# Optimization experiments

Measured on AMD Instinct MI355X. Metric: run time of the kernel, lower is better.

## Reference

```python
import jax, jax.numpy as jnp
import numpy as np

L, B, D_IN, H = 1024, 64, 512, 512


def setup_inputs() -> dict:
    key = jax.random.key(0)
    ks = jax.random.split(key, 9)
    s = 1.0 / np.sqrt(H)
    inp = {
        "inputs": jax.random.normal(ks[0], (L, B, D_IN), dtype=jnp.float32),
        # canonical chain tree: node at step t is node t (left child = t-1)
        "indexes": jnp.broadcast_to(jnp.arange(L, dtype=jnp.int32)[:, None], (L, B)),
        # gate linears: ih has bias, lhh/rhh do not (per nn.Linear defs)
        "W_gih": jax.random.uniform(ks[1], (5 * H, D_IN), jnp.float32, -s, s),
        "b_gih": jax.random.uniform(ks[2], (5 * H,), jnp.float32, -s, s),
        "W_glhh": jax.random.uniform(ks[3], (5 * H, H), jnp.float32, -s, s),
        "W_grhh": jax.random.uniform(ks[4], (5 * H, H), jnp.float32, -s, s),
        "W_cih": jax.random.uniform(ks[5], (H, D_IN), jnp.float32, -s, s),
        "b_cih": jax.random.uniform(ks[6], (H,), jnp.float32, -s, s),
        "W_clhh": jax.random.uniform(ks[7], (H, H), jnp.float32, -s, s),
        "W_crhh": jax.random.uniform(ks[8], (H, H), jnp.float32, -s, s),
    }
    return inp


def _tree_gru(inputs, W_gih, b_gih, W_glhh, W_grhh, W_cih, b_cih, W_clhh, W_crhh):
    # chain tree: left_child_h = previous hidden, right_child_h = 0 (leaf side)
    batch = inputs.shape[1]
    hidden = W_clhh.shape[0]
    h0 = jnp.zeros((batch, hidden), inputs.dtype)

    def step(h_prev, x_t):
        left = h_prev
        right = jnp.zeros_like(h_prev)
        gates = jax.nn.sigmoid(
            x_t @ W_gih.T + b_gih + left @ W_glhh.T + right @ W_grhh.T
        )
        rl, rr, zl, zr, z = jnp.split(gates, 5, axis=1)
        cell = jnp.tanh(
            x_t @ W_cih.T + b_cih + (rl * left) @ W_clhh.T + (rr * right) @ W_crhh.T
        )
        h = zl * left + zr * right + z * cell  # node_forward hidden
        return h, h

    _, hs = jax.lax.scan(step, h0, inputs)  # hs: [L, B, H]
    outputs = jnp.transpose(hs, (1, 0, 2))  # [B, L, H], batch-first like original
    output_t = jnp.zeros((batch, hidden), inputs.dtype)  # original returns zeros
    return outputs, output_t


def reference(inputs, indexes, W_gih, b_gih, W_glhh, W_grhh, W_cih, b_cih,
              W_clhh, W_crhh):
    del indexes  # chain ordering: indexes[step, b] == step
    return _tree_gru(inputs, W_gih, b_gih, W_glhh, W_grhh,
                     W_cih, b_cih, W_clhh, W_crhh)
```

## Files before the change

kernel.cpp:

```cpp
#include <hip/hip_runtime.h>
#include <hip/hip_bf16.h>
#include <stdint.h>

typedef __bf16 bf16;
typedef __bf16 bf16x8 __attribute__((ext_vector_type(8)));
typedef __bf16 bf16x4 __attribute__((ext_vector_type(4)));
typedef float f32x16 __attribute__((ext_vector_type(16)));
typedef float f32x4 __attribute__((ext_vector_type(4)));

#define LL 1024
#define BB 64
#define HH 512
#define NR 8
#define NC 16
#define NWG (NR + NC)
#define NPROD 32
#define NLAUNCH (NWG + NPROD)
#define WSLOT 16
#define MFMA32(a, b, c) __builtin_amdgcn_mfma_f32_32x32x16_bf16(a, b, c, 0, 0, 0)

#define OFF_X      ((size_t)0)
#define OFF_WGSEL  ((size_t)67108864)
#define OFF_WCIH   ((size_t)68681728)
#define OFF_WHHZZ  ((size_t)69206016)
#define OFF_HBUF   ((size_t)70254592)
#define OFF_A2     ((size_t)70385664)
#define OFF_CTR    ((size_t)70516736)
#define OFF_XS     ((size_t)70517760)

static __device__ __forceinline__ float sigm(float x) {
  return 1.0f / (1.0f + __expf(-x));
}
static __device__ __forceinline__ float tanhx(float x) {
  x = fminf(15.0f, fmaxf(-15.0f, x));
  float e = __expf(2.0f * x);
  return (e - 1.0f) / (e + 1.0f);
}

static __device__ __forceinline__ unsigned ld_stamp(const unsigned* p) {
  unsigned s;
  asm volatile("global_load_dword %0, %1, off sc0 sc1\n\ts_waitcnt vmcnt(0)"
               : "=v"(s) : "v"(p) : "memory");
  return s;
}
static __device__ __forceinline__ void st_stamp(unsigned* p, unsigned v) {
  asm volatile("global_store_dword %0, %1, off sc0 sc1" :: "v"(p), "v"(v) : "memory");
}
static __device__ __forceinline__ void ld_frag(const bf16* p, bf16x8& d) {
  asm volatile("global_load_dwordx4 %0, %1, off sc0 sc1" : "=v"(d) : "v"(p) : "memory");
}
static __device__ __forceinline__ void ld_frag_c(const bf16* p, bf16x8& d) {
  asm volatile("global_load_dwordx4 %0, %1, off" : "=v"(d) : "v"(p) : "memory");
}
static __device__ __forceinline__ void ld_f4(const float* p, f32x4& d) {
  asm volatile("global_load_dwordx4 %0, %1, off sc0 sc1" : "=v"(d) : "v"(p) : "memory");
}
static __device__ __forceinline__ void st_f4(float* p, f32x4 v) {
  asm volatile("global_store_dwordx4 %0, %1, off sc0 sc1" :: "v"(p), "v"(v) : "memory");
}
static __device__ __forceinline__ void ld_u16(const bf16* p, unsigned& d) {
  asm volatile("global_load_ushort %0, %1, off sc0 sc1" : "=v"(d) : "v"(p) : "memory");
}
static __device__ __forceinline__ void st_u16(bf16* p, unsigned v) {
  asm volatile("global_store_short %0, %1, off sc0 sc1" :: "v"(p), "v"(v) : "memory");
}
#define VWAIT(n) do { asm volatile("s_waitcnt vmcnt(" #n ")" ::: "memory"); \
                      __builtin_amdgcn_sched_barrier(0); } while (0)

static __device__ __forceinline__ bf16x8 ldsfrag(const bf16* w, int i, int k) {
  unsigned byte = ((unsigned)i << 10) + ((unsigned)k << 1);
  byte ^= ((unsigned)(i & 7) << 4);
  return *(const bf16x8*)((const char*)w + byte);
}

__global__ __launch_bounds__(256) void k_cvt_x(const float* __restrict__ in,
                                               bf16* __restrict__ o) {
  size_t i = ((size_t)blockIdx.x * 256 + threadIdx.x) * 4;
  float4 f = *(const float4*)(in + i);
  bf16x4 v;
  v[0] = (bf16)f.x; v[1] = (bf16)f.y; v[2] = (bf16)f.z; v[3] = (bf16)f.w;
  *(bf16x4*)(o + i) = v;
}

__global__ __launch_bounds__(256) void k_cvt_w(const float* __restrict__ wgih,
                                               const float* __restrict__ wcf,
                                               const float* __restrict__ wglhh,
                                               bf16* __restrict__ wgsel,
                                               bf16* __restrict__ wcb,
                                               bf16* __restrict__ whhzz) {
  int i = blockIdx.x * 256 + threadIdx.x;
  const int NQ1 = (1536 * 512) / 4;
  const int NQ2 = (512 * 512) / 4;
  const float* s;
  bf16* d;
  if (i < NQ1) {
    int e = i * 4;
    int p = e >> 9, k = e & 511;
    int src = (p < 512) ? p : ((p < 1024) ? (1024 + p - 512) : (2048 + p - 1024));
    s = wgih + (size_t)src * 512 + k;
    d = wgsel + (size_t)p * 512 + k;
  } else if (i < NQ1 + NQ2) {
    int e = (i - NQ1) * 4;
    int n = e >> 9, k = e & 511;
    s = wcf + (size_t)n * 512 + k;
    d = wcb + (size_t)n * 512 + k;
  } else {
    int e = (i - NQ1 - NQ2) * 4;
    int q = e >> 9, k = e & 511;
    int src = (q < 512) ? (1024 + q) : (2048 + q - 512);
    s = wglhh + (size_t)src * 512 + k;
    d = whhzz + (size_t)q * 512 + k;
  }
  float4 f = *(const float4*)s;
  bf16x4 v;
  v[0] = (bf16)f.x; v[1] = (bf16)f.y; v[2] = (bf16)f.z; v[3] = (bf16)f.w;
  *(bf16x4*)d = v;
}

__global__ __launch_bounds__(256) void k_main(
    const bf16* __restrict__ xbf, const bf16* __restrict__ wgsel,
    const bf16* __restrict__ wcb, const bf16* __restrict__ whhzz,
    const float* __restrict__ wglhh, const float* __restrict__ wclhh,
    const float* __restrict__ bg, const float* __restrict__ bc,
    float* __restrict__ out, bf16* __restrict__ hbuf,
    bf16* __restrict__ a2buf, float* __restrict__ xs,
    unsigned* __restrict__ ctrs) {
  __shared__ __align__(16) char smem[64 * 1024];
  bf16* wlds = (bf16*)smem;
  float* zlzs = (float*)(smem + 32 * 1024);

  const int wg = blockIdx.x, tid = threadIdx.x;
  const int lane = tid & 63, wave = tid >> 6;
  const int lr = lane & 31, kq = (lane >> 5) * 8;
  unsigned* astamp = ctrs;
  unsigned* hstamp = ctrs + 16;
  unsigned* xstamp = ctrs + 64;

  if (wg >= NWG) {
    const int gx = (wg - NWG) * 4 + wave;
    const int proj = gx >> 5;
    const int m0 = 32 * ((gx >> 4) & 1);
    const int col = (gx & 15) * 32 + lr;
    float bias;
    const bf16* wb;
    if (proj == 0)      { bias = bg[col];        wb = wgsel + (size_t)col * HH; }
    else if (proj == 1) { bias = bg[1024 + col]; wb = wgsel + (size_t)(512 + col) * HH; }
    else if (proj == 2) { bias = bg[2048 + col]; wb = wgsel + (size_t)(1024 + col) * HH; }
    else                { bias = bc[col];        wb = wcb + (size_t)col * HH; }
    wb += kq;
    float* xsl = xs + ((size_t)gx * 64 + lane) * 16;
    for (int t = 0; t < LL; ++t) {
      if (t >= WSLOT) {
        const unsigned* sp = hstamp + (lane & 15);
        while (__any((int)(ld_stamp(sp) < (unsigned)(t - WSLOT + 1)))) {}
      }
      f32x16 a;
      #pragma unroll
      for (int r = 0; r < 16; ++r) a[r] = bias;
      const bf16* xa = xbf + (size_t)t * (BB * HH) + (size_t)(m0 + lr) * HH + kq;
      #pragma unroll 4
      for (int kk = 0; kk < 32; ++kk)
        a = MFMA32(*(const bf16x8*)(xa + kk * 16), *(const bf16x8*)(wb + kk * 16), a);
      float* dst = xsl + (size_t)(t & (WSLOT - 1)) * (128 * 64 * 16);
      f32x4 v0, v1, v2, v3;
      #pragma unroll
      for (int e = 0; e < 4; ++e) { v0[e] = a[e]; v1[e] = a[4 + e]; v2[e] = a[8 + e]; v3[e] = a[12 + e]; }
      st_f4(dst, v0); st_f4(dst + 4, v1); st_f4(dst + 8, v2); st_f4(dst + 12, v3);
      asm volatile("s_waitcnt vmcnt(0)" ::: "memory");
      if (lane == 0) st_stamp(xstamp + gx, (unsigned)(t + 1));
    }
    return;
  }
  __builtin_amdgcn_s_setprio(1);

  if (wg < NR) {
    const int m0 = 32 * (wave & 1);
    const int lc = 32 * (wave >> 1) + lr;
    const int p = wg * 64 + lc;
    const int mrow = m0 + 4 * (lane >> 5);
    const int gx = (wave & 1) * 16 + 2 * wg + (wave >> 1);

    for (int u = tid; u < 64 * 64; u += 256) {
      int i = u >> 6, k8 = (u & 63) << 3;
      const float* s = wglhh + (size_t)(wg * 64 + i) * HH + k8;
      bf16x8 v;
      #pragma unroll
      for (int j = 0; j < 8; ++j) v[j] = (bf16)s[j];
      unsigned byte = ((unsigned)i << 10) + ((unsigned)k8 << 1);
      byte ^= ((unsigned)(i & 7) << 4);
      *(bf16x8*)((char*)wlds + byte) = v;
    }
    __syncthreads();

    for (int t = 1; t < LL; ++t) {
      {
        const unsigned* sp = hstamp + (lane & 15);
        unsigned tgt = (unsigned)t;
        if (lane == 16) { sp = xstamp + gx; tgt = (unsigned)(t + 1); }
        while (__any((int)(ld_stamp(sp) < tgt))) {}
      }
      __builtin_amdgcn_sched_barrier(0);
      const float* xsp = xs + (((size_t)(t & (WSLOT - 1)) * 128 + gx) * 64 + lane) * 16;
      f32x4 xv0, xv1, xv2, xv3;
      ld_f4(xsp, xv0); ld_f4(xsp + 4, xv1); ld_f4(xsp + 8, xv2); ld_f4(xsp + 12, xv3);
      const bf16* hs = hbuf + (size_t)((t - 1) & 1) * (BB * HH);
      const bf16* ha = hs + (size_t)(m0 + lr) * HH + kq;
      bf16x8 fA[8], fB[8];
      unsigned hv[16];
      f32x16 acc;
      #pragma unroll
      for (int r = 0; r < 16; ++r) acc[r] = 0.0f;
      #pragma unroll
      for (int j = 0; j < 8; ++j) ld_frag(ha + j * 16, fA[j]);
      #pragma unroll
      for (int j = 0; j < 8; ++j) ld_frag(ha + (8 + j) * 16, fB[j]);
      VWAIT(8);
      #pragma unroll
      for (int j = 0; j < 8; ++j) acc = MFMA32(fA[j], ldsfrag(wlds, lc, j * 16 + kq), acc);
      #pragma unroll
      for (int j = 0; j < 8; ++j) ld_frag(ha + (16 + j) * 16, fA[j]);
      VWAIT(8);
      #pragma unroll
      for (int j = 0; j < 8; ++j) acc = MFMA32(fB[j], ldsfrag(wlds, lc, (8 + j) * 16 + kq), acc);
      #pragma unroll
      for (int j = 0; j < 8; ++j) ld_frag(ha + (24 + j) * 16, fB[j]);
      #pragma unroll
      for (int r = 0; r < 16; ++r) {
        int m = mrow + (r & 3) + 8 * (r >> 2);
        ld_u16(hs + (size_t)m * HH + p, hv[r]);
      }
      VWAIT(24);
      #pragma unroll
      for (int j = 0; j < 8; ++j) acc = MFMA32(fA[j], ldsfrag(wlds, lc, (16 + j) * 16 + kq), acc);
      VWAIT(16);
      #pragma unroll
      for (int j = 0; j < 8; ++j) acc = MFMA32(fB[j], ldsfrag(wlds, lc, (24 + j) * 16 + kq), acc);
      VWAIT(0);
      bf16* ad = a2buf + (size_t)(t & 1) * (BB * HH);
      #pragma unroll
      for (int r = 0; r < 16; ++r) {
        int m = mrow + (r & 3) + 8 * (r >> 2);
        float xadd = (r < 4) ? xv0[r & 3] : (r < 8) ? xv1[r & 3]
                   : (r < 12) ? xv2[r & 3] : xv3[r & 3];
        float gg = sigm(acc[r] + xadd);
        float hp = __builtin_bit_cast(float, hv[r] << 16);
        bf16 a = (bf16)(gg * hp);
        st_u16(ad + (size_t)m * HH + p, (unsigned)__builtin_bit_cast(unsigned short, a));
      }
      asm volatile("s_waitcnt vmcnt(0)" ::: "memory");
      __syncthreads();
      if (tid == 0) st_stamp(astamp + wg, (unsigned)(t + 1));
    }
  } else {
    const int cj = wg - NR;
    const int n = cj * 32 + lr;
    const bool crit = (wave < 2);
    const int m0 = crit ? 32 * wave : 32 * (wave - 2);
    const int mrow = m0 + 4 * (lane >> 5);
    const int Mq = (m0 >> 5) * 16;
    const int gc = 96 + Mq + cj;
    const int gzl = 32 + Mq + cj;
    const int gz = 64 + Mq + cj;

    for (int u = tid; u < 32 * 64; u += 256) {
      int i = u >> 6, k8 = (u & 63) << 3;
      const float* s = wclhh + (size_t)(cj * 32 + i) * HH + k8;
      bf16x8 v;
      #pragma unroll
      for (int j = 0; j < 8; ++j) v[j] = (bf16)s[j];
      unsigned byte = ((unsigned)i << 10) + ((unsigned)k8 << 1);
      byte ^= ((unsigned)(i & 7) << 4);
      *(bf16x8*)((char*)wlds + byte) = v;
    }
    __syncthreads();

    float hreg[16];
    #pragma unroll
    for (int r = 0; r < 16; ++r) hreg[r] = 0.0f;

    for (int t = 0; t < LL; ++t) {
      if (crit) {
        f32x16 acc, acc1;
        #pragma unroll
        for (int r = 0; r < 16; ++r) { acc[r] = 0.0f; acc1[r] = 0.0f; }
        f32x4 xv0, xv1, xv2, xv3;
        if (t > 0) {
          {
            const unsigned* sp = astamp + (lane & 7);
            unsigned tgt = (unsigned)(t + 1);
            if (lane == 8) sp = xstamp + gc;
            while (__any((int)(ld_stamp(sp) < tgt))) {}
          }
          __builtin_amdgcn_sched_barrier(0);
          const float* xsp = xs + (((size_t)(t & (WSLOT - 1)) * 128 + gc) * 64 + lane) * 16;
          ld_f4(xsp, xv0); ld_f4(xsp + 4, xv1); ld_f4(xsp + 8, xv2); ld_f4(xsp + 12, xv3);
          const bf16* aa = a2buf + (size_t)(t & 1) * (BB * HH) + (size_t)(m0 + lr) * HH + kq;
          bf16x8 fA[8], fB[8];
          #pragma unroll
          for (int j = 0; j < 8; ++j) ld_frag(aa + j * 16, fA[j]);
          #pragma unroll
          for (int j = 0; j < 8; ++j) ld_frag(aa + (8 + j) * 16, fB[j]);
          VWAIT(8);
          #pragma unroll
          for (int j = 0; j < 8; ++j) {
            if (j & 1) acc1 = MFMA32(fA[j], ldsfrag(wlds, lr, j * 16 + kq), acc1);
            else       acc  = MFMA32(fA[j], ldsfrag(wlds, lr, j * 16 + kq), acc);
          }
          #pragma unroll
          for (int j = 0; j < 8; ++j) ld_frag(aa + (16 + j) * 16, fA[j]);
          VWAIT(8);
          #pragma unroll
          for (int j = 0; j < 8; ++j) {
            if (j & 1) acc1 = MFMA32(fB[j], ldsfrag(wlds, lr, (8 + j) * 16 + kq), acc1);
            else       acc  = MFMA32(fB[j], ldsfrag(wlds, lr, (8 + j) * 16 + kq), acc);
          }
          #pragma unroll
          for (int j = 0; j < 8; ++j) ld_frag(aa + (24 + j) * 16, fB[j]);
          VWAIT(8);
          #pragma unroll
          for (int j = 0; j < 8; ++j) {
            if (j & 1) acc1 = MFMA32(fA[j], ldsfrag(wlds, lr, (16 + j) * 16 + kq), acc1);
            else       acc  = MFMA32(fA[j], ldsfrag(wlds, lr, (16 + j) * 16 + kq), acc);
          }
          VWAIT(0);
          #pragma unroll
          for (int j = 0; j < 8; ++j) {
            if (j & 1) acc1 = MFMA32(fB[j], ldsfrag(wlds, lr, (24 + j) * 16 + kq), acc1);
            else       acc  = MFMA32(fB[j], ldsfrag(wlds, lr, (24 + j) * 16 + kq), acc);
          }
        } else {
          {
            const unsigned* sp = xstamp + gc;
            while (__any((int)(ld_stamp(sp) < 1u))) {}
          }
          __builtin_amdgcn_sched_barrier(0);
          const float* xsp = xs + ((size_t)gc * 64 + lane) * 16;
          ld_f4(xsp, xv0); ld_f4(xsp + 4, xv1); ld_f4(xsp + 8, xv2); ld_f4(xsp + 12, xv3);
          VWAIT(0);
        }
        #pragma unroll
        for (int r = 0; r < 16; ++r) {
          float xadd = (r < 4) ? xv0[r & 3] : (r < 8) ? xv1[r & 3]
                     : (r < 12) ? xv2[r & 3] : xv3[r & 3];
          acc[r] += acc1[r] + xadd;
        }
        __syncthreads();
        bf16* hd = hbuf + (size_t)(t & 1) * (BB * HH);
        #pragma unroll
        for (int r = 0; r < 16; ++r) {
          int m = mrow + (r & 3) + 8 * (r >> 2);
          float zlv = zlzs[m * 32 + lr];
          float zv = zlzs[2048 + m * 32 + lr];
          float h = zlv * hreg[r] + zv * tanhx(acc[r]);
          hreg[r] = h;
          bf16 hb = (bf16)h;
          st_u16(hd + (size_t)m * HH + n, (unsigned)__builtin_bit_cast(unsigned short, hb));
        }
        asm volatile("s_waitcnt vmcnt(0)" ::: "memory");
      } else {
        f32x16 azl, az;
        #pragma unroll
        for (int r = 0; r < 16; ++r) { azl[r] = 0.0f; az[r] = 0.0f; }
        f32x4 l0, l1, l2, l3, z0, z1, z2, z3;
        if (t > 0) {
          {
            const unsigned* sp = hstamp + (lane & 15);
            unsigned tgt = (unsigned)t;
            if (lane == 16) { sp = xstamp + gzl; tgt = (unsigned)(t + 1); }
            if (lane == 17) { sp = xstamp + gz; tgt = (unsigned)(t + 1); }
            while (__any((int)(ld_stamp(sp) < tgt))) {}
          }
          __builtin_amdgcn_sched_barrier(0);
          const float* xl = xs + (((size_t)(t & (WSLOT - 1)) * 128 + gzl) * 64 + lane) * 16;
          const float* xz = xs + (((size_t)(t & (WSLOT - 1)) * 128 + gz) * 64 + lane) * 16;
          ld_f4(xl, l0); ld_f4(xl + 4, l1); ld_f4(xl + 8, l2); ld_f4(xl + 12, l3);
          ld_f4(xz, z0); ld_f4(xz + 4, z1); ld_f4(xz + 8, z2); ld_f4(xz + 12, z3);
          const bf16* hsA = hbuf + (size_t)((t - 1) & 1) * (BB * HH) + (size_t)(m0 + lr) * HH + kq;
          const bf16* bl = whhzz + (size_t)n * HH + kq;
          const bf16* bz = whhzz + (size_t)(512 + n) * HH + kq;
          bf16x8 A[2][4], Wl[2][4], Wz[2][4];
          #pragma unroll
          for (int j = 0; j < 4; ++j) {
            ld_frag(hsA + j * 16, A[0][j]);
            ld_frag_c(bl + j * 16, Wl[0][j]);
            ld_frag_c(bz + j * 16, Wz[0][j]);
          }
          #pragma unroll
          for (int b = 0; b < 8; ++b) {
            const int s = b & 1, ns = s ^ 1;
            if (b < 7) {
              #pragma unroll
              for (int j = 0; j < 4; ++j) {
                ld_frag(hsA + ((b + 1) * 4 + j) * 16, A[ns][j]);
                ld_frag_c(bl + ((b + 1) * 4 + j) * 16, Wl[ns][j]);
                ld_frag_c(bz + ((b + 1) * 4 + j) * 16, Wz[ns][j]);
              }
              VWAIT(12);
            } else {
              VWAIT(0);
            }
            #pragma unroll
            for (int j = 0; j < 4; ++j) {
              azl = MFMA32(A[s][j], Wl[s][j], azl);
              az = MFMA32(A[s][j], Wz[s][j], az);
            }
          }
        } else {
          {
            const unsigned* sp = xstamp + ((lane & 1) ? gz : gzl);
            while (__any((int)(ld_stamp(sp) < 1u))) {}
          }
          __builtin_amdgcn_sched_barrier(0);
          const float* xl = xs + ((size_t)gzl * 64 + lane) * 16;
          const float* xz = xs + ((size_t)gz * 64 + lane) * 16;
          ld_f4(xl, l0); ld_f4(xl + 4, l1); ld_f4(xl + 8, l2); ld_f4(xl + 12, l3);
          ld_f4(xz, z0); ld_f4(xz + 4, z1); ld_f4(xz + 8, z2); ld_f4(xz + 12, z3);
          VWAIT(0);
        }
        #pragma unroll
        for (int r = 0; r < 16; ++r) {
          int m = mrow + (r & 3) + 8 * (r >> 2);
          float xla = (r < 4) ? l0[r & 3] : (r < 8) ? l1[r & 3]
                    : (r < 12) ? l2[r & 3] : l3[r & 3];
          float xza = (r < 4) ? z0[r & 3] : (r < 8) ? z1[r & 3]
                    : (r < 12) ? z2[r & 3] : z3[r & 3];
          zlzs[m * 32 + lr] = sigm(azl[r] + xla);
          zlzs[2048 + m * 32 + lr] = sigm(az[r] + xza);
        }
        __syncthreads();
      }
      __syncthreads();
      if (tid == 0) st_stamp(hstamp + cj, (unsigned)(t + 1));
      if (crit) {
        #pragma unroll
        for (int r = 0; r < 16; ++r) {
          int m = mrow + (r & 3) + 8 * (r >> 2);
          out[(size_t)m * (LL * HH) + (size_t)t * HH + n] = hreg[r];
        }
      }
    }
  }
}

extern "C" void kernel_launch(void* const* d_in, const int* in_sizes, int n_in,
                              void* d_out, int out_size, void* d_ws, size_t ws_size,
                              hipStream_t stream) {
  (void)in_sizes; (void)n_in; (void)out_size; (void)ws_size;
  const float* x     = (const float*)d_in[0];
  const float* wgih  = (const float*)d_in[2];
  const float* bg    = (const float*)d_in[3];
  const float* wglhh = (const float*)d_in[4];
  const float* wcihf = (const float*)d_in[6];
  const float* bc    = (const float*)d_in[7];
  const float* wclhh = (const float*)d_in[8];
  float* out = (float*)d_out;

  char* ws = (char*)d_ws;
  bf16* xbf     = (bf16*)(ws + OFF_X);
  bf16* wgsel   = (bf16*)(ws + OFF_WGSEL);
  bf16* wcb     = (bf16*)(ws + OFF_WCIH);
  bf16* whhzz   = (bf16*)(ws + OFF_WHHZZ);
  bf16* hbuf    = (bf16*)(ws + OFF_HBUF);
  bf16* a2buf   = (bf16*)(ws + OFF_A2);
  float* xsb    = (float*)(ws + OFF_XS);
  unsigned* ctr = (unsigned*)(ws + OFF_CTR);

  hipMemsetAsync(ctr, 0, 1024, stream);
  hipMemsetAsync(out + (size_t)BB * LL * HH, 0, (size_t)BB * HH * sizeof(float), stream);

  k_cvt_x<<<dim3(32768), dim3(256), 0, stream>>>(x, xbf);
  k_cvt_w<<<dim3(1536), dim3(256), 0, stream>>>(wgih, wcihf, wglhh, wgsel, wcb, whhzz);
  k_main<<<dim3(NLAUNCH), dim3(256), 0, stream>>>(xbf, wgsel, wcb, whhzz, wglhh, wclhh,
                                                  bg, bc, out, hbuf, a2buf, xsb, ctr);
}
```

Baseline: 14.29 ms.

## Replace stamp-counter handshakes with per-element tagged hidden-state words

The hidden state and the gated product are now stored as 32-bit words, with the bf16 value in the high half and the step number in the low half. Consumers poll the data itself and retry only the fragments whose tags are stale, which replaces the separate stamp counters and the workgroup barrier plus stamp store on the producer side. This is meant to cut the cross-workgroup synchronisation latency on the serial recurrence path. In exchange it doubles the buffer footprint and global traffic per step, and adds unpacking ALU work and retry loops.

```diff
diff --git a/kernel.cpp b/kernel.cpp
--- a/kernel.cpp
+++ b/kernel.cpp
@@ -7,6 +7,8 @@
 typedef __bf16 bf16x4 __attribute__((ext_vector_type(4)));
 typedef float f32x16 __attribute__((ext_vector_type(16)));
 typedef float f32x4 __attribute__((ext_vector_type(4)));
+typedef unsigned u32;
+typedef unsigned u32x4 __attribute__((ext_vector_type(4)));
 
 #define LL 1024
 #define BB 64
@@ -24,9 +26,9 @@
 #define OFF_WCIH   ((size_t)68681728)
 #define OFF_WHHZZ  ((size_t)69206016)
 #define OFF_HBUF   ((size_t)70254592)
-#define OFF_A2     ((size_t)70385664)
-#define OFF_CTR    ((size_t)70516736)
-#define OFF_XS     ((size_t)70517760)
+#define OFF_A2     ((size_t)70516736)
+#define OFF_CTR    ((size_t)70778880)
+#define OFF_XS     ((size_t)70780928)
 
 static __device__ __forceinline__ float sigm(float x) {
   return 1.0f / (1.0f + __expf(-x));
@@ -46,8 +48,14 @@
 static __device__ __forceinline__ void st_stamp(unsigned* p, unsigned v) {
   asm volatile("global_store_dword %0, %1, off sc0 sc1" :: "v"(p), "v"(v) : "memory");
 }
-static __device__ __forceinline__ void ld_frag(const bf16* p, bf16x8& d) {
+static __device__ __forceinline__ void ld_d4(const u32* p, u32x4& d) {
   asm volatile("global_load_dwordx4 %0, %1, off sc0 sc1" : "=v"(d) : "v"(p) : "memory");
+}
+static __device__ __forceinline__ void ld_d1(const u32* p, u32& d) {
+  asm volatile("global_load_dword %0, %1, off sc0 sc1" : "=v"(d) : "v"(p) : "memory");
+}
+static __device__ __forceinline__ void st_d1(u32* p, u32 v) {
+  asm volatile("global_store_dword %0, %1, off sc0 sc1" :: "v"(p), "v"(v) : "memory");
 }
 static __device__ __forceinline__ void ld_frag_c(const bf16* p, bf16x8& d) {
   asm volatile("global_load_dwordx4 %0, %1, off" : "=v"(d) : "v"(p) : "memory");
@@ -58,14 +66,33 @@
 static __device__ __forceinline__ void st_f4(float* p, f32x4 v) {
   asm volatile("global_store_dwordx4 %0, %1, off sc0 sc1" :: "v"(p), "v"(v) : "memory");
 }
-static __device__ __forceinline__ void ld_u16(const bf16* p, unsigned& d) {
-  asm volatile("global_load_ushort %0, %1, off sc0 sc1" : "=v"(d) : "v"(p) : "memory");
-}
-static __device__ __forceinline__ void st_u16(bf16* p, unsigned v) {
-  asm volatile("global_store_short %0, %1, off sc0 sc1" :: "v"(p), "v"(v) : "memory");
-}
 #define VWAIT(n) do { asm volatile("s_waitcnt vmcnt(" #n ")" ::: "memory"); \
                       __builtin_amdgcn_sched_barrier(0); } while (0)
+
+#define PK2(a, b) (((a) >> 16) | ((b) & 0xFFFF0000u))
+static __device__ __forceinline__ bf16x8 frag_of(u32x4 a, u32x4 b) {
+  u32x4 p;
+  p[0] = PK2(a[0], a[1]); p[1] = PK2(a[2], a[3]);
+  p[2] = PK2(b[0], b[1]); p[3] = PK2(b[2], b[3]);
+  return __builtin_bit_cast(bf16x8, p);
+}
+static __device__ __forceinline__ bool bad4(u32x4 w, u32 et) {
+  return ((w[0] & 0xFFFFu) != et) | ((w[1] & 0xFFFFu) != et) |
+         ((w[2] & 0xFFFFu) != et) | ((w[3] & 0xFFFFu) != et);
+}
+static __device__ __forceinline__ void issue4(const u32* base, int g, u32x4* b) {
+  #pragma unroll
+  for (int j = 0; j < 4; ++j) {
+    ld_d4(base + (g * 4 + j) * 16, b[2 * j]);
+    ld_d4(base + (g * 4 + j) * 16 + 4, b[2 * j + 1]);
+  }
+}
+static __device__ __forceinline__ bool badbank(const u32x4* b, u32 et) {
+  bool bad = false;
+  #pragma unroll
+  for (int i = 0; i < 8; ++i) bad |= bad4(b[i], et);
+  return bad;
+}
 
 static __device__ __forceinline__ bf16x8 ldsfrag(const bf16* w, int i, int k) {
   unsigned byte = ((unsigned)i << 10) + ((unsigned)k << 1);
@@ -122,8 +149,8 @@
     const bf16* __restrict__ wcb, const bf16* __restrict__ whhzz,
     const float* __restrict__ wglhh, const float* __restrict__ wclhh,
     const float* __restrict__ bg, const float* __restrict__ bc,
-    float* __restrict__ out, bf16* __restrict__ hbuf,
-    bf16* __restrict__ a2buf, float* __restrict__ xs,
+    float* __restrict__ out, u32* __restrict__ hbuf32,
+    u32* __restrict__ a2buf32, float* __restrict__ xs,
     unsigned* __restrict__ ctrs) {
   __shared__ __align__(16) char smem[64 * 1024];
   bf16* wlds = (bf16*)smem;
@@ -132,7 +159,6 @@
   const int wg = blockIdx.x, tid = threadIdx.x;
   const int lane = tid & 63, wave = tid >> 6;
   const int lr = lane & 31, kq = (lane >> 5) * 8;
-  unsigned* astamp = ctrs;
   unsigned* hstamp = ctrs + 16;
   unsigned* xstamp = ctrs + 64;
 
@@ -193,63 +219,76 @@
     __syncthreads();
 
     for (int t = 1; t < LL; ++t) {
-      {
-        const unsigned* sp = hstamp + (lane & 15);
-        unsigned tgt = (unsigned)t;
-        if (lane == 16) { sp = xstamp + gx; tgt = (unsigned)(t + 1); }
-        while (__any((int)(ld_stamp(sp) < tgt))) {}
-      }
-      __builtin_amdgcn_sched_barrier(0);
+      const int par = (t - 1) & 1;
+      const u32 et = (u32)t;
+      const u32* hb = hbuf32 + (size_t)par * 32768 + (size_t)(m0 + lr) * 512 + kq;
+      const u32* hB = hbuf32 + (size_t)par * 32768;
+      u32x4 b0[8], b1[8];
+      u32 hv[16];
+      f32x16 acc;
+      #pragma unroll
+      for (int r = 0; r < 16; ++r) acc[r] = 0.0f;
+      f32x4 xv0, xv1, xv2, xv3;
+      bool xok = false;
+      for (;;) {
+        issue4(hb, 0, b0);
+        #pragma unroll
+        for (int r = 0; r < 16; ++r) {
+          int m = mrow + (r & 3) + 8 * (r >> 2);
+          ld_d1(hB + (size_t)m * 512 + p, hv[r]);
+        }
+        u32 xst = 0;
+        if (!xok) ld_d1((const u32*)(xstamp + gx), xst);
+        VWAIT(0);
+        if (!xok) xok = (xst >= (u32)(t + 1));
+        bool bad = badbank(b0, et);
+        #pragma unroll
+        for (int r = 0; r < 16; ++r) bad |= ((hv[r] & 0xFFFFu) != et);
+        if (!__any((int)bad)) break;
+      }
+      while (!xok) {
+        u32 xst;
+        ld_d1((const u32*)(xstamp + gx), xst);
+        VWAIT(0);
+        xok = (xst >= (u32)(t + 1));
+      }
       const float* xsp = xs + (((size_t)(t & (WSLOT - 1)) * 128 + gx) * 64 + lane) * 16;
-      f32x4 xv0, xv1, xv2, xv3;
       ld_f4(xsp, xv0); ld_f4(xsp + 4, xv1); ld_f4(xsp + 8, xv2); ld_f4(xsp + 12, xv3);
-      const bf16* hs = hbuf + (size_t)((t - 1) & 1) * (BB * HH);
-      const bf16* ha = hs + (size_t)(m0 + lr) * HH + kq;
-      bf16x8 fA[8], fB[8];
-      unsigned hv[16];
-      f32x16 acc;
-      #pragma unroll
-      for (int r = 0; r < 16; ++r) acc[r] = 0.0f;
-      #pragma unroll
-      for (int j = 0; j < 8; ++j) ld_frag(ha + j * 16, fA[j]);
-      #pragma unroll
-      for (int j = 0; j < 8; ++j) ld_frag(ha + (8 + j) * 16, fB[j]);
+      issue4(hb, 1, b1);
       VWAIT(8);
       #pragma unroll
-      for (int j = 0; j < 8; ++j) acc = MFMA32(fA[j], ldsfrag(wlds, lc, j * 16 + kq), acc);
-      #pragma unroll
-      for (int j = 0; j < 8; ++j) ld_frag(ha + (16 + j) * 16, fA[j]);
-      VWAIT(8);
-      #pragma unroll
-      for (int j = 0; j < 8; ++j) acc = MFMA32(fB[j], ldsfrag(wlds, lc, (8 + j) * 16 + kq), acc);
-      #pragma unroll
-      for (int j = 0; j < 8; ++j) ld_frag(ha + (24 + j) * 16, fB[j]);
-      #pragma unroll
-      for (int r = 0; r < 16; ++r) {
-        int m = mrow + (r & 3) + 8 * (r >> 2);
-        ld_u16(hs + (size_t)m * HH + p, hv[r]);
-      }
-      VWAIT(24);
-      #pragma unroll
-      for (int j = 0; j < 8; ++j) acc = MFMA32(fA[j], ldsfrag(wlds, lc, (16 + j) * 16 + kq), acc);
-      VWAIT(16);
-      #pragma unroll
-      for (int j = 0; j < 8; ++j) acc = MFMA32(fB[j], ldsfrag(wlds, lc, (24 + j) * 16 + kq), acc);
+      for (int j = 0; j < 4; ++j)
+        acc = MFMA32(frag_of(b0[2 * j], b0[2 * j + 1]), ldsfrag(wlds, lc, j * 16 + kq), acc);
+      #pragma unroll
+      for (int g = 1; g <= 6; ++g) {
+        u32x4* cur = (g & 1) ? b1 : b0;
+        u32x4* nxt = (g & 1) ? b0 : b1;
+        issue4(hb, g + 1, nxt);
+        VWAIT(8);
+        while (__any((int)badbank(cur, et))) { VWAIT(0); issue4(hb, g, cur); VWAIT(0); }
+        #pragma unroll
+        for (int j = 0; j < 4; ++j)
+          acc = MFMA32(frag_of(cur[2 * j], cur[2 * j + 1]),
+                       ldsfrag(wlds, lc, (4 * g + j) * 16 + kq), acc);
+      }
       VWAIT(0);
-      bf16* ad = a2buf + (size_t)(t & 1) * (BB * HH);
+      while (__any((int)badbank(b1, et))) { issue4(hb, 7, b1); VWAIT(0); }
+      #pragma unroll
+      for (int j = 0; j < 4; ++j)
+        acc = MFMA32(frag_of(b1[2 * j], b1[2 * j + 1]),
+                     ldsfrag(wlds, lc, (28 + j) * 16 + kq), acc);
+      u32* ad = a2buf32 + (size_t)(t & 1) * 32768;
       #pragma unroll
       for (int r = 0; r < 16; ++r) {
         int m = mrow + (r & 3) + 8 * (r >> 2);
         float xadd = (r < 4) ? xv0[r & 3] : (r < 8) ? xv1[r & 3]
                    : (r < 12) ? xv2[r & 3] : xv3[r & 3];
         float gg = sigm(acc[r] + xadd);
-        float hp = __builtin_bit_cast(float, hv[r] << 16);
-        bf16 a = (bf16)(gg * hp);
-        st_u16(ad + (size_t)m * HH + p, (unsigned)__builtin_bit_cast(unsigned short, a));
-      }
-      asm volatile("s_waitcnt vmcnt(0)" ::: "memory");
-      __syncthreads();
-      if (tid == 0) st_stamp(astamp + wg, (unsigned)(t + 1));
+        float hp = __builtin_bit_cast(float, hv[r] & 0xFFFF0000u);
+        bf16 av = (bf16)(gg * hp);
+        u32 w = ((u32)__builtin_bit_cast(unsigned short, av) << 16) | (u32)(t + 1);
+        st_d1(ad + (size_t)m * 512 + p, w);
+      }
     }
   } else {
     const int cj = wg - NR;
@@ -280,59 +319,57 @@
 
     for (int t = 0; t < LL; ++t) {
       if (crit) {
-        f32x16 acc, acc1;
-        #pragma unroll
-        for (int r = 0; r < 16; ++r) { acc[r] = 0.0f; acc1[r] = 0.0f; }
+        f32x16 acc;
+        #pragma unroll
+        for (int r = 0; r < 16; ++r) acc[r] = 0.0f;
         f32x4 xv0, xv1, xv2, xv3;
         if (t > 0) {
-          {
-            const unsigned* sp = astamp + (lane & 7);
-            unsigned tgt = (unsigned)(t + 1);
-            if (lane == 8) sp = xstamp + gc;
-            while (__any((int)(ld_stamp(sp) < tgt))) {}
-          }
-          __builtin_amdgcn_sched_barrier(0);
+          const u32 et = (u32)(t + 1);
+          const u32* ab = a2buf32 + (size_t)(t & 1) * 32768 + (size_t)(m0 + lr) * 512 + kq;
+          u32x4 b0[8], b1[8];
+          bool xok = false;
+          for (;;) {
+            issue4(ab, 0, b0);
+            u32 xst = 0;
+            if (!xok) ld_d1((const u32*)(xstamp + gc), xst);
+            VWAIT(0);
+            if (!xok) xok = (xst >= (u32)(t + 1));
+            if (!__any((int)badbank(b0, et))) break;
+          }
+          while (!xok) {
+            u32 xst;
+            ld_d1((const u32*)(xstamp + gc), xst);
+            VWAIT(0);
+            xok = (xst >= (u32)(t + 1));
+          }
           const float* xsp = xs + (((size_t)(t & (WSLOT - 1)) * 128 + gc) * 64 + lane) * 16;
           ld_f4(xsp, xv0); ld_f4(xsp + 4, xv1); ld_f4(xsp + 8, xv2); ld_f4(xsp + 12, xv3);
-          const bf16* aa = a2buf + (size_t)(t & 1) * (BB * HH) + (size_t)(m0 + lr) * HH + kq;
-          bf16x8 fA[8], fB[8];
-          #pragma unroll
-          for (int j = 0; j < 8; ++j) ld_frag(aa + j * 16, fA[j]);
-          #pragma unroll
-          for (int j = 0; j < 8; ++j) ld_frag(aa + (8 + j) * 16, fB[j]);
+          issue4(ab, 1, b1);
           VWAIT(8);
           #pragma unroll
-          for (int j = 0; j < 8; ++j) {
-            if (j & 1) acc1 = MFMA32(fA[j], ldsfrag(wlds, lr, j * 16 + kq), acc1);
-            else       acc  = MFMA32(fA[j], ldsfrag(wlds, lr, j * 16 + kq), acc);
-          }
+          for (int j = 0; j < 4; ++j)
+            acc = MFMA32(frag_of(b0[2 * j], b0[2 * j + 1]), ldsfrag(wlds, lr, j * 16 + kq), acc);
           #pragma unroll
-          for (int j = 0; j < 8; ++j) ld_frag(aa + (16 + j) * 16, fA[j]);
-          VWAIT(8);
+          for (int g = 1; g <= 6; ++g) {
+            u32x4* cur = (g & 1) ? b1 : b0;
+            u32x4* nxt = (g & 1) ? b0 : b1;
+            issue4(ab, g + 1, nxt);
+            VWAIT(8);
+            while (__any((int)badbank(cur, et))) { VWAIT(0); issue4(ab, g, cur); VWAIT(0); }
+            #pragma unroll
+            for (int j = 0; j < 4; ++j)
+              acc = MFMA32(frag_of(cur[2 * j], cur[2 * j + 1]),
+                           ldsfrag(wlds, lr, (4 * g + j) * 16 + kq), acc);
+          }
+          VWAIT(0);
+          while (__any((int)badbank(b1, et))) { issue4(ab, 7, b1); VWAIT(0); }
           #pragma unroll
-          for (int j = 0; j < 8; ++j) {
-            if (j & 1) acc1 = MFMA32(fB[j], ldsfrag(wlds, lr, (8 + j) * 16 + kq), acc1);
-            else       acc  = MFMA32(fB[j], ldsfrag(wlds, lr, (8 + j) * 16 + kq), acc);
-          }
-          #pragma unroll
-          for (int j = 0; j < 8; ++j) ld_frag(aa + (24 + j) * 16, fB[j]);
-          VWAIT(8);
-          #pragma unroll
-          for (int j = 0; j < 8; ++j) {
-            if (j & 1) acc1 = MFMA32(fA[j], ldsfrag(wlds, lr, (16 + j) * 16 + kq), acc1);
-            else       acc  = MFMA32(fA[j], ldsfrag(wlds, lr, (16 + j) * 16 + kq), acc);
-          }
-          VWAIT(0);
-          #pragma unroll
-          for (int j = 0; j < 8; ++j) {
-            if (j & 1) acc1 = MFMA32(fB[j], ldsfrag(wlds, lr, (24 + j) * 16 + kq), acc1);
-            else       acc  = MFMA32(fB[j], ldsfrag(wlds, lr, (24 + j) * 16 + kq), acc);
-          }
+          for (int j = 0; j < 4; ++j)
+            acc = MFMA32(frag_of(b1[2 * j], b1[2 * j + 1]),
+                         ldsfrag(wlds, lr, (28 + j) * 16 + kq), acc);
         } else {
-          {
-            const unsigned* sp = xstamp + gc;
-            while (__any((int)(ld_stamp(sp) < 1u))) {}
-          }
+          const unsigned* sp = xstamp + gc;
+          while (__any((int)(ld_stamp(sp) < 1u))) {}
           __builtin_amdgcn_sched_barrier(0);
           const float* xsp = xs + ((size_t)gc * 64 + lane) * 16;
           ld_f4(xsp, xv0); ld_f4(xsp + 4, xv1); ld_f4(xsp + 8, xv2); ld_f4(xsp + 12, xv3);
@@ -342,10 +379,10 @@
         for (int r = 0; r < 16; ++r) {
           float xadd = (r < 4) ? xv0[r & 3] : (r < 8) ? xv1[r & 3]
                      : (r < 12) ? xv2[r & 3] : xv3[r & 3];
-          acc[r] += acc1[r] + xadd;
+          acc[r] += xadd;
         }
         __syncthreads();
-        bf16* hd = hbuf + (size_t)(t & 1) * (BB * HH);
+        u32* hd = hbuf32 + (size_t)(t & 1) * 32768;
         #pragma unroll
         for (int r = 0; r < 16; ++r) {
           int m = mrow + (r & 3) + 8 * (r >> 2);
@@ -353,8 +390,9 @@
           float zv = zlzs[2048 + m * 32 + lr];
           float h = zlv * hreg[r] + zv * tanhx(acc[r]);
           hreg[r] = h;
-          bf16 hb = (bf16)h;
-          st_u16(hd + (size_t)m * HH + n, (unsigned)__builtin_bit_cast(unsigned short, hb));
+          bf16 hb16 = (bf16)h;
+          u32 w = ((u32)__builtin_bit_cast(unsigned short, hb16) << 16) | (u32)(t + 1);
+          st_d1(hd + (size_t)m * 512 + n, w);
         }
         asm volatile("s_waitcnt vmcnt(0)" ::: "memory");
       } else {
@@ -371,40 +409,43 @@
             while (__any((int)(ld_stamp(sp) < tgt))) {}
           }
           __builtin_amdgcn_sched_barrier(0);
-          const float* xl = xs + (((size_t)(t & (WSLOT - 1)) * 128 + gzl) * 64 + lane) * 16;
-          const float* xz = xs + (((size_t)(t & (WSLOT - 1)) * 128 + gz) * 64 + lane) * 16;
-          ld_f4(xl, l0); ld_f4(xl + 4, l1); ld_f4(xl + 8, l2); ld_f4(xl + 12, l3);
-          ld_f4(xz, z0); ld_f4(xz + 4, z1); ld_f4(xz + 8, z2); ld_f4(xz + 12, z3);
-          const bf16* hsA = hbuf + (size_t)((t - 1) & 1) * (BB * HH) + (size_t)(m0 + lr) * HH + kq;
+          const u32* hA = hbuf32 + (size_t)((t - 1) & 1) * 32768 + (size_t)(m0 + lr) * 512 + kq;
           const bf16* bl = whhzz + (size_t)n * HH + kq;
           const bf16* bz = whhzz + (size_t)(512 + n) * HH + kq;
-          bf16x8 A[2][4], Wl[2][4], Wz[2][4];
+          u32x4 hb2[2][8];
+          bf16x8 Wl[2][4], Wz[2][4];
+          issue4(hA, 0, hb2[0]);
           #pragma unroll
           for (int j = 0; j < 4; ++j) {
-            ld_frag(hsA + j * 16, A[0][j]);
             ld_frag_c(bl + j * 16, Wl[0][j]);
             ld_frag_c(bz + j * 16, Wz[0][j]);
           }
           #pragma unroll
-          for (int b = 0; b < 8; ++b) {
-            const int s = b & 1, ns = s ^ 1;
-            if (b < 7) {
+          for (int g = 0; g < 8; ++g) {
+            const int s = g & 1, ns = s ^ 1;
+            if (g < 7) {
+              issue4(hA, g + 1, hb2[ns]);
               #pragma unroll
               for (int j = 0; j < 4; ++j) {
-                ld_frag(hsA + ((b + 1) * 4 + j) * 16, A[ns][j]);
-                ld_frag_c(bl + ((b + 1) * 4 + j) * 16, Wl[ns][j]);
-                ld_frag_c(bz + ((b + 1) * 4 + j) * 16, Wz[ns][j]);
+                ld_frag_c(bl + ((g + 1) * 4 + j) * 16, Wl[ns][j]);
+                ld_frag_c(bz + ((g + 1) * 4 + j) * 16, Wz[ns][j]);
               }
-              VWAIT(12);
+              VWAIT(16);
             } else {
               VWAIT(0);
             }
             #pragma unroll
             for (int j = 0; j < 4; ++j) {
-              azl = MFMA32(A[s][j], Wl[s][j], azl);
-              az = MFMA32(A[s][j], Wz[s][j], az);
+              bf16x8 fr = frag_of(hb2[s][2 * j], hb2[s][2 * j + 1]);
+              azl = MFMA32(fr, Wl[s][j], azl);
+              az = MFMA32(fr, Wz[s][j], az);
             }
           }
+          const float* xl = xs + (((size_t)(t & (WSLOT - 1)) * 128 + gzl) * 64 + lane) * 16;
+          const float* xz = xs + (((size_t)(t & (WSLOT - 1)) * 128 + gz) * 64 + lane) * 16;
+          ld_f4(xl, l0); ld_f4(xl + 4, l1); ld_f4(xl + 8, l2); ld_f4(xl + 12, l3);
+          ld_f4(xz, z0); ld_f4(xz + 4, z1); ld_f4(xz + 8, z2); ld_f4(xz + 12, z3);
+          VWAIT(0);
         } else {
           {
             const unsigned* sp = xstamp + ((lane & 1) ? gz : gzl);
@@ -460,8 +501,8 @@
   bf16* wgsel   = (bf16*)(ws + OFF_WGSEL);
   bf16* wcb     = (bf16*)(ws + OFF_WCIH);
   bf16* whhzz   = (bf16*)(ws + OFF_WHHZZ);
-  bf16* hbuf    = (bf16*)(ws + OFF_HBUF);
-  bf16* a2buf   = (bf16*)(ws + OFF_A2);
+  u32* hbuf32   = (u32*)(ws + OFF_HBUF);
+  u32* a2buf32  = (u32*)(ws + OFF_A2);
   float* xsb    = (float*)(ws + OFF_XS);
   unsigned* ctr = (unsigned*)(ws + OFF_CTR);
 
@@ -471,5 +512,5 @@
   k_cvt_x<<<dim3(32768), dim3(256), 0, stream>>>(x, xbf);
   k_cvt_w<<<dim3(1536), dim3(256), 0, stream>>>(wgih, wcihf, wglhh, wgsel, wcb, whhzz);
   k_main<<<dim3(NLAUNCH), dim3(256), 0, stream>>>(xbf, wgsel, wcb, whhzz, wglhh, wclhh,
-                                                  bg, bc, out, hbuf, a2buf, xsb, ctr);
-}
+                                                  bg, bc, out, hbuf32, a2buf32, xsb, ctr);
+}
```

Measured after the change: 20.96 ms. 1.47x slower.

## Stage recurrent hidden and gated activations through LDS before MFMA

Applied to the files above, without the earlier changes.

The reset-gate workgroups now cooperatively copy the whole previous hidden state (64x512 bf16) into a swizzled LDS buffer. The MFMA A-fragments and the per-element h_prev values are then read from LDS, replacing per-lane strided global loads and scalar ushort loads. The cell workgroups' critical waves similarly stage their 32-row slice of a2 into per-wave LDS regions before a single-accumulator MFMA loop. Shared memory grows to 128KB, and the staging adds a full load-then-store round plus a barrier on the serial critical path, removing the earlier overlap of global loads with MFMAs.

```diff
diff --git a/kernel.cpp b/kernel.cpp
--- a/kernel.cpp
+++ b/kernel.cpp
@@ -57,9 +57,6 @@
 }
 static __device__ __forceinline__ void st_f4(float* p, f32x4 v) {
   asm volatile("global_store_dwordx4 %0, %1, off sc0 sc1" :: "v"(p), "v"(v) : "memory");
-}
-static __device__ __forceinline__ void ld_u16(const bf16* p, unsigned& d) {
-  asm volatile("global_load_ushort %0, %1, off sc0 sc1" : "=v"(d) : "v"(p) : "memory");
 }
 static __device__ __forceinline__ void st_u16(bf16* p, unsigned v) {
   asm volatile("global_store_short %0, %1, off sc0 sc1" :: "v"(p), "v"(v) : "memory");
@@ -125,9 +122,8 @@
     float* __restrict__ out, bf16* __restrict__ hbuf,
     bf16* __restrict__ a2buf, float* __restrict__ xs,
     unsigned* __restrict__ ctrs) {
-  __shared__ __align__(16) char smem[64 * 1024];
+  __shared__ __align__(16) char smem[128 * 1024];
   bf16* wlds = (bf16*)smem;
-  float* zlzs = (float*)(smem + 32 * 1024);
 
   const int wg = blockIdx.x, tid = threadIdx.x;
   const int lane = tid & 63, wave = tid >> 6;
@@ -174,6 +170,7 @@
   __builtin_amdgcn_s_setprio(1);
 
   if (wg < NR) {
+    bf16* hstage = (bf16*)(smem + 65536);
     const int m0 = 32 * (wave & 1);
     const int lc = 32 * (wave >> 1) + lr;
     const int p = wg * 64 + lc;
@@ -204,48 +201,43 @@
       f32x4 xv0, xv1, xv2, xv3;
       ld_f4(xsp, xv0); ld_f4(xsp + 4, xv1); ld_f4(xsp + 8, xv2); ld_f4(xsp + 12, xv3);
       const bf16* hs = hbuf + (size_t)((t - 1) & 1) * (BB * HH);
-      const bf16* ha = hs + (size_t)(m0 + lr) * HH + kq;
-      bf16x8 fA[8], fB[8];
-      unsigned hv[16];
+      #pragma unroll
+      for (int rnd = 0; rnd < 2; ++rnd) {
+        bf16x8 tmp[8];
+        #pragma unroll
+        for (int j = 0; j < 8; ++j) {
+          int u = rnd * 2048 + j * 256 + tid;
+          ld_frag(hs + (size_t)(u >> 6) * 512 + ((u & 63) << 3), tmp[j]);
+        }
+        VWAIT(0);
+        #pragma unroll
+        for (int j = 0; j < 8; ++j) {
+          int u = rnd * 2048 + j * 256 + tid;
+          unsigned byte = ((unsigned)(u >> 6) << 10) + ((unsigned)((u & 63) << 3) << 1);
+          byte ^= ((unsigned)((u >> 6) & 7) << 4);
+          *(bf16x8*)((char*)hstage + byte) = tmp[j];
+        }
+      }
+      __syncthreads();
       f32x16 acc;
       #pragma unroll
       for (int r = 0; r < 16; ++r) acc[r] = 0.0f;
-      #pragma unroll
-      for (int j = 0; j < 8; ++j) ld_frag(ha + j * 16, fA[j]);
-      #pragma unroll
-      for (int j = 0; j < 8; ++j) ld_frag(ha + (8 + j) * 16, fB[j]);
-      VWAIT(8);
-      #pragma unroll
-      for (int j = 0; j < 8; ++j) acc = MFMA32(fA[j], ldsfrag(wlds, lc, j * 16 + kq), acc);
-      #pragma unroll
-      for (int j = 0; j < 8; ++j) ld_frag(ha + (16 + j) * 16, fA[j]);
-      VWAIT(8);
-      #pragma unroll
-      for (int j = 0; j < 8; ++j) acc = MFMA32(fB[j], ldsfrag(wlds, lc, (8 + j) * 16 + kq), acc);
-      #pragma unroll
-      for (int j = 0; j < 8; ++j) ld_frag(ha + (24 + j) * 16, fB[j]);
+      #pragma unroll 8
+      for (int kk = 0; kk < 32; ++kk)
+        acc = MFMA32(ldsfrag(hstage, m0 + lr, kk * 16 + kq),
+                     ldsfrag(wlds, lc, kk * 16 + kq), acc);
+      bf16* ad = a2buf + (size_t)(t & 1) * (BB * HH);
       #pragma unroll
       for (int r = 0; r < 16; ++r) {
         int m = mrow + (r & 3) + 8 * (r >> 2);
-        ld_u16(hs + (size_t)m * HH + p, hv[r]);
-      }
-      VWAIT(24);
-      #pragma unroll
-      for (int j = 0; j < 8; ++j) acc = MFMA32(fA[j], ldsfrag(wlds, lc, (16 + j) * 16 + kq), acc);
-      VWAIT(16);
-      #pragma unroll
-      for (int j = 0; j < 8; ++j) acc = MFMA32(fB[j], ldsfrag(wlds, lc, (24 + j) * 16 + kq), acc);
-      VWAIT(0);
-      bf16* ad = a2buf + (size_t)(t & 1) * (BB * HH);
-      #pragma unroll
-      for (int r = 0; r < 16; ++r) {
-        int m = mrow + (r & 3) + 8 * (r >> 2);
+        unsigned hb_ = ((unsigned)m << 10) + ((unsigned)p << 1);
+        hb_ ^= ((unsigned)(m & 7) << 4);
+        float hp = (float)*(const bf16*)((const char*)hstage + hb_);
         float xadd = (r < 4) ? xv0[r & 3] : (r < 8) ? xv1[r & 3]
                    : (r < 12) ? xv2[r & 3] : xv3[r & 3];
         float gg = sigm(acc[r] + xadd);
-        float hp = __builtin_bit_cast(float, hv[r] << 16);
-        bf16 a = (bf16)(gg * hp);
-        st_u16(ad + (size_t)m * HH + p, (unsigned)__builtin_bit_cast(unsigned short, a));
+        bf16 av = (bf16)(gg * hp);
+        st_u16(ad + (size_t)m * HH + p, (unsigned)__builtin_bit_cast(unsigned short, av));
       }
       asm volatile("s_waitcnt vmcnt(0)" ::: "memory");
       __syncthreads();
@@ -253,6 +245,7 @@
     }
   } else {
     const int cj = wg - NR;
+    float* zlzs = (float*)(smem + 32768);
     const int n = cj * 32 + lr;
     const bool crit = (wave < 2);
     const int m0 = crit ? 32 * wave : 32 * (wave - 2);
@@ -280,9 +273,9 @@
 
     for (int t = 0; t < LL; ++t) {
       if (crit) {
-        f32x16 acc, acc1;
-        #pragma unroll
-        for (int r = 0; r < 16; ++r) { acc[r] = 0.0f; acc1[r] = 0.0f; }
+        f32x16 acc;
+        #pragma unroll
+        for (int r = 0; r < 16; ++r) acc[r] = 0.0f;
         f32x4 xv0, xv1, xv2, xv3;
         if (t > 0) {
           {
@@ -294,40 +287,31 @@
           __builtin_amdgcn_sched_barrier(0);
           const float* xsp = xs + (((size_t)(t & (WSLOT - 1)) * 128 + gc) * 64 + lane) * 16;
           ld_f4(xsp, xv0); ld_f4(xsp + 4, xv1); ld_f4(xsp + 8, xv2); ld_f4(xsp + 12, xv3);
-          const bf16* aa = a2buf + (size_t)(t & 1) * (BB * HH) + (size_t)(m0 + lr) * HH + kq;
-          bf16x8 fA[8], fB[8];
+          bf16* myst = (bf16*)(smem + 49152 + wave * 32768);
+          const bf16* ab = a2buf + (size_t)(t & 1) * (BB * HH) + (size_t)m0 * HH;
           #pragma unroll
-          for (int j = 0; j < 8; ++j) ld_frag(aa + j * 16, fA[j]);
-          #pragma unroll
-          for (int j = 0; j < 8; ++j) ld_frag(aa + (8 + j) * 16, fB[j]);
-          VWAIT(8);
-          #pragma unroll
-          for (int j = 0; j < 8; ++j) {
-            if (j & 1) acc1 = MFMA32(fA[j], ldsfrag(wlds, lr, j * 16 + kq), acc1);
-            else       acc  = MFMA32(fA[j], ldsfrag(wlds, lr, j * 16 + kq), acc);
-          }
-          #pragma unroll
-          for (int j = 0; j < 8; ++j) ld_frag(aa + (16 + j) * 16, fA[j]);
-          VWAIT(8);
-          #pragma unroll
-          for (int j = 0; j < 8; ++j) {
-            if (j & 1) acc1 = MFMA32(fB[j], ldsfrag(wlds, lr, (8 + j) * 16 + kq), acc1);
-            else       acc  = MFMA32(fB[j], ldsfrag(wlds, lr, (8 + j) * 16 + kq), acc);
-          }
-          #pragma unroll
-          for (int j = 0; j < 8; ++j) ld_frag(aa + (24 + j) * 16, fB[j]);
-          VWAIT(8);
-          #pragma unroll
-          for (int j = 0; j < 8; ++j) {
-            if (j & 1) acc1 = MFMA32(fA[j], ldsfrag(wlds, lr, (16 + j) * 16 + kq), acc1);
-            else       acc  = MFMA32(fA[j], ldsfrag(wlds, lr, (16 + j) * 16 + kq), acc);
-          }
-          VWAIT(0);
-          #pragma unroll
-          for (int j = 0; j < 8; ++j) {
-            if (j & 1) acc1 = MFMA32(fB[j], ldsfrag(wlds, lr, (24 + j) * 16 + kq), acc1);
-            else       acc  = MFMA32(fB[j], ldsfrag(wlds, lr, (24 + j) * 16 + kq), acc);
-          }
+          for (int rnd = 0; rnd < 4; ++rnd) {
+            bf16x8 tmp[8];
+            #pragma unroll
+            for (int j = 0; j < 8; ++j) {
+              int u = rnd * 512 + j * 64 + lane;
+              ld_frag(ab + (size_t)(u >> 6) * 512 + ((u & 63) << 3), tmp[j]);
+            }
+            VWAIT(0);
+            #pragma unroll
+            for (int j = 0; j < 8; ++j) {
+              int u = rnd * 512 + j * 64 + lane;
+              unsigned byte = ((unsigned)(u >> 6) << 10) + ((unsigned)((u & 63) << 3) << 1);
+              byte ^= ((unsigned)((u >> 6) & 7) << 4);
+              *(bf16x8*)((char*)myst + byte) = tmp[j];
+            }
+          }
+          asm volatile("s_waitcnt lgkmcnt(0)" ::: "memory");
+          __builtin_amdgcn_sched_barrier(0);
+          #pragma unroll 8
+          for (int kk = 0; kk < 32; ++kk)
+            acc = MFMA32(ldsfrag(myst, lr, kk * 16 + kq),
+                         ldsfrag(wlds, lr, kk * 16 + kq), acc);
         } else {
           {
             const unsigned* sp = xstamp + gc;
@@ -342,7 +326,7 @@
         for (int r = 0; r < 16; ++r) {
           float xadd = (r < 4) ? xv0[r & 3] : (r < 8) ? xv1[r & 3]
                      : (r < 12) ? xv2[r & 3] : xv3[r & 3];
-          acc[r] += acc1[r] + xadd;
+          acc[r] += xadd;
         }
         __syncthreads();
         bf16* hd = hbuf + (size_t)(t & 1) * (BB * HH);
@@ -353,8 +337,8 @@
           float zv = zlzs[2048 + m * 32 + lr];
           float h = zlv * hreg[r] + zv * tanhx(acc[r]);
           hreg[r] = h;
-          bf16 hb = (bf16)h;
-          st_u16(hd + (size_t)m * HH + n, (unsigned)__builtin_bit_cast(unsigned short, hb));
+          bf16 hb16 = (bf16)h;
+          st_u16(hd + (size_t)m * HH + n, (unsigned)__builtin_bit_cast(unsigned short, hb16));
         }
         asm volatile("s_waitcnt vmcnt(0)" ::: "memory");
       } else {
```

Measured after the change: 12.80 ms. -10.5%, faster.
